# Kernel tuning notes

Hardware: AMD Instinct MI355X
Metric: run time of the kernel (lower is better)

The kernel has to match this reference:

```python
import jax, jax.numpy as jnp
import numpy as np

N_NODES = 50000
N_EDGES = 800000
FEAT_DIM = 1024
EMBED_DIM = 128


def setup_inputs() -> dict:
    key = jax.random.key(0)
    k_x, k_w, k_r, k_c, k_v = jax.random.split(key, 5)
    x = jax.random.normal(k_x, (N_NODES, FEAT_DIM), dtype=jnp.float32)
    # xavier-uniform equivalent for weight [embed_dim, feat_dim]
    limit = float(np.sqrt(6.0 / (EMBED_DIM + FEAT_DIM)))
    weight = jax.random.uniform(k_w, (EMBED_DIM, FEAT_DIM), dtype=jnp.float32,
                                minval=-limit, maxval=limit)
    # sparse adjacency in COO form (row = destination, col = source)
    adj_row = jax.random.randint(k_r, (N_EDGES,), 0, N_NODES, dtype=jnp.int32)
    adj_col = jax.random.randint(k_c, (N_EDGES,), 0, N_NODES, dtype=jnp.int32)
    adj_vals = jax.random.uniform(k_v, (N_EDGES,), dtype=jnp.float32)
    return {"x": x, "weight": weight, "adj_row": adj_row,
            "adj_col": adj_col, "adj_vals": adj_vals}


def reference(x, weight, adj_row, adj_col, adj_vals):
    # Fused GeMM-SpMM: out = A @ (x @ W^T)
    h = jnp.einsum('nf,ef->ne', x, weight)          # [N, embed_dim] dense GEMM
    msgs = adj_vals[:, None] * h[adj_col]           # gather source rows, scale by edge weight
    out = jax.ops.segment_sum(msgs, adj_row, num_segments=N_NODES)  # scatter-add to dest rows
    return out
```

## Files before the change

### kernel.cpp

```cpp
#include <hip/hip_runtime.h>
#include <hip/hip_bf16.h>

#define FEAT 1024
#define EMBED 128
#define CAP 64
#define OVF_CAP 4096

typedef __attribute__((ext_vector_type(8))) short short8;
typedef __attribute__((ext_vector_type(4))) float floatx4;

__device__ inline ushort f2bf(float f) {
    __hip_bfloat16 h = __float2bfloat16(f);
    return *reinterpret_cast<ushort*>(&h);
}
__device__ inline float bfbits_lo(uint u) {
    uint v = u << 16; return *reinterpret_cast<float*>(&v);
}
__device__ inline float bfbits_hi(uint u) {
    uint v = u & 0xffff0000u; return *reinterpret_cast<float*>(&v);
}

__device__ inline void async_copy16(const void* g, void* l) {
    __builtin_amdgcn_global_load_lds(
        (const __attribute__((address_space(1))) void*)g,
        (__attribute__((address_space(3))) void*)l, 16, 0, 0);
}

__global__ void swizzle_weight_kernel(const float* __restrict__ w,
                                      ushort* __restrict__ wbs) {
    int gid = blockIdx.x * blockDim.x + threadIdx.x;
    int l = gid & 63;
    int t = (gid >> 6) & 7;
    int s = gid >> 9;
    int row = t * 16 + (l & 15);
    int col = s * 32 + (l >> 4) * 8;
    const float* src = w + (size_t)row * FEAT + col;
    float4 v0 = *(const float4*)(src);
    float4 v1 = *(const float4*)(src + 4);
    short8 o;
    o[0] = f2bf(v0.x); o[1] = f2bf(v0.y); o[2] = f2bf(v0.z); o[3] = f2bf(v0.w);
    o[4] = f2bf(v1.x); o[5] = f2bf(v1.y); o[6] = f2bf(v1.z); o[7] = f2bf(v1.w);
    *(short8*)(wbs + (size_t)gid * 8) = o;
}

__launch_bounds__(256, 2)
__global__ void gemm_bucket_kernel(const float* __restrict__ x,
                                   const ushort* __restrict__ wbs,
                                   ushort* __restrict__ hb, int n_nodes,
                                   const int* __restrict__ adj_row,
                                   const int* __restrict__ adj_col,
                                   const float* __restrict__ adj_vals,
                                   int* __restrict__ cnt,
                                   int2* __restrict__ bucket,
                                   int* __restrict__ ovf_cnt,
                                   int* __restrict__ ovf_list,
                                   int n_edges, int gemm_blocks) {
    __shared__ ushort lds[2][16384];

    if (blockIdx.x >= gemm_blocks) {
        int e = (blockIdx.x - gemm_blocks) * 256 + threadIdx.x;
        if (e < n_edges) {
            int r = adj_row[e];
            int slot = atomicAdd(&cnt[r], 1);
            if (slot < CAP) {
                bucket[(size_t)r * CAP + slot] =
                    make_int2(adj_col[e], __float_as_int(adj_vals[e]));
            } else {
                int oi = atomicAdd(ovf_cnt, 1);
                if (oi < OVF_CAP) ovf_list[oi] = e;
            }
        }
        return;
    }

    const int lane = threadIdx.x & 63;
    const int wave = threadIdx.x >> 6;
    const int q    = lane >> 4;
    const int m    = lane & 15;
    const int base = blockIdx.x * 128 + wave * 32;

    int row0 = base + m;
    int row1 = base + 16 + m;
    int r0l = row0 < n_nodes ? row0 : (n_nodes - 1);
    int r1l = row1 < n_nodes ? row1 : (n_nodes - 1);
    const float* xp0 = x + (size_t)r0l * FEAT + q * 8;
    const float* xp1 = x + (size_t)r1l * FEAT + q * 8;

    const char* wb = (const char*)wbs;
    const size_t stage_src_off = (size_t)(wave * 8 * 64 + lane) * 16;
    const int    stage_dst_off = wave * 8192;

    {
        const char* src = wb + stage_src_off;
        char* dst = (char*)lds[0] + stage_dst_off;
#pragma unroll
        for (int k = 0; k < 8; ++k)
            async_copy16(src + k * 1024, dst + k * 1024);
    }

    float4 A[4][4];
#pragma unroll
    for (int u = 0; u < 4; ++u) {
        A[u][0] = *(const float4*)(xp0 + u * 32);
        A[u][1] = *(const float4*)(xp0 + u * 32 + 4);
        A[u][2] = *(const float4*)(xp1 + u * 32);
        A[u][3] = *(const float4*)(xp1 + u * 32 + 4);
    }

    floatx4 acc[2][8];
#pragma unroll
    for (int rf = 0; rf < 2; ++rf)
#pragma unroll
        for (int t = 0; t < 8; ++t) acc[rf][t] = (floatx4)(0.0f);

    __syncthreads();

    for (int c = 0; c < 8; ++c) {
        const ushort* buf = lds[c & 1];
        if (c < 7) {
            const char* src = wb + (size_t)(c + 1) * 32768 + stage_src_off;
            char* dst = (char*)lds[(c + 1) & 1] + stage_dst_off;
#pragma unroll
            for (int k = 0; k < 8; ++k)
                async_copy16(src + k * 1024, dst + k * 1024);
        }
#pragma unroll
        for (int u = 0; u < 4; ++u) {
            const ushort* bs = buf + u * 4096 + lane * 8;
            short8 bf[8];
#pragma unroll
            for (int t = 0; t < 8; ++t) bf[t] = *(const short8*)(bs + t * 512);

            short8 af0, af1;
            af0[0] = f2bf(A[u][0].x); af0[1] = f2bf(A[u][0].y);
            af0[2] = f2bf(A[u][0].z); af0[3] = f2bf(A[u][0].w);
            af0[4] = f2bf(A[u][1].x); af0[5] = f2bf(A[u][1].y);
            af0[6] = f2bf(A[u][1].z); af0[7] = f2bf(A[u][1].w);
            af1[0] = f2bf(A[u][2].x); af1[1] = f2bf(A[u][2].y);
            af1[2] = f2bf(A[u][2].z); af1[3] = f2bf(A[u][2].w);
            af1[4] = f2bf(A[u][3].x); af1[5] = f2bf(A[u][3].y);
            af1[6] = f2bf(A[u][3].z); af1[7] = f2bf(A[u][3].w);

            if (c < 7) {
                const float* p0 = xp0 + (c + 1) * 128;
                const float* p1 = xp1 + (c + 1) * 128;
                if (u == 1) {
#pragma unroll
                    for (int uu = 0; uu < 2; ++uu) {
                        A[uu][0] = *(const float4*)(p0 + uu * 32);
                        A[uu][1] = *(const float4*)(p0 + uu * 32 + 4);
                        A[uu][2] = *(const float4*)(p1 + uu * 32);
                        A[uu][3] = *(const float4*)(p1 + uu * 32 + 4);
                    }
                } else if (u == 3) {
#pragma unroll
                    for (int uu = 2; uu < 4; ++uu) {
                        A[uu][0] = *(const float4*)(p0 + uu * 32);
                        A[uu][1] = *(const float4*)(p0 + uu * 32 + 4);
                        A[uu][2] = *(const float4*)(p1 + uu * 32);
                        A[uu][3] = *(const float4*)(p1 + uu * 32 + 4);
                    }
                }
            }
#pragma unroll
            for (int t = 0; t < 8; ++t) {
                acc[0][t] = __builtin_amdgcn_mfma_f32_16x16x32_bf16(af0, bf[t], acc[0][t], 0, 0, 0);
                acc[1][t] = __builtin_amdgcn_mfma_f32_16x16x32_bf16(af1, bf[t], acc[1][t], 0, 0, 0);
            }
        }
        __syncthreads();
    }

#pragma unroll
    for (int rf = 0; rf < 2; ++rf) {
#pragma unroll
        for (int t = 0; t < 8; ++t) {
#pragma unroll
            for (int r = 0; r < 4; ++r) {
                int rr = base + rf * 16 + q * 4 + r;
                if (rr < n_nodes)
                    hb[(size_t)rr * EMBED + t * 16 + m] = f2bf(acc[rf][t][r]);
            }
        }
    }
}

__launch_bounds__(256)
__global__ void gather_kernel(const int* __restrict__ cnt,
                              const int2* __restrict__ bucket,
                              const ushort* __restrict__ hb,
                              const int* __restrict__ ovf_cnt,
                              const int* __restrict__ ovf_list,
                              const int* __restrict__ adj_row,
                              const int* __restrict__ adj_col,
                              const float* __restrict__ adj_vals,
                              float* __restrict__ out, int n_nodes) {
    int node = __builtin_amdgcn_readfirstlane(blockIdx.x * 4 + (threadIdx.x >> 6));
    if (node >= n_nodes) return;
    int lane = threadIdx.x & 63;
    int c_raw = cnt[node];
    int c = c_raw > CAP ? CAP : c_raw;
    const int2* bp = bucket + (size_t)node * CAP;
    const ushort* hl = hb + lane * 2;

    float accx = 0.0f, accy = 0.0f;
    int j = 0;
    for (; j + 8 <= c; j += 8) {
        int4 e01 = *(const int4*)(bp + j);
        int4 e23 = *(const int4*)(bp + j + 2);
        int4 e45 = *(const int4*)(bp + j + 4);
        int4 e67 = *(const int4*)(bp + j + 6);
        uint u0 = *(const uint*)(hl + (size_t)e01.x * EMBED);
        uint u1 = *(const uint*)(hl + (size_t)e01.z * EMBED);
        uint u2 = *(const uint*)(hl + (size_t)e23.x * EMBED);
        uint u3 = *(const uint*)(hl + (size_t)e23.z * EMBED);
        uint u4 = *(const uint*)(hl + (size_t)e45.x * EMBED);
        uint u5 = *(const uint*)(hl + (size_t)e45.z * EMBED);
        uint u6 = *(const uint*)(hl + (size_t)e67.x * EMBED);
        uint u7 = *(const uint*)(hl + (size_t)e67.z * EMBED);
        float w0 = __int_as_float(e01.y), w1 = __int_as_float(e01.w);
        float w2 = __int_as_float(e23.y), w3 = __int_as_float(e23.w);
        float w4 = __int_as_float(e45.y), w5 = __int_as_float(e45.w);
        float w6 = __int_as_float(e67.y), w7 = __int_as_float(e67.w);
        accx = fmaf(w0, bfbits_lo(u0), accx);  accy = fmaf(w0, bfbits_hi(u0), accy);
        accx = fmaf(w1, bfbits_lo(u1), accx);  accy = fmaf(w1, bfbits_hi(u1), accy);
        accx = fmaf(w2, bfbits_lo(u2), accx);  accy = fmaf(w2, bfbits_hi(u2), accy);
        accx = fmaf(w3, bfbits_lo(u3), accx);  accy = fmaf(w3, bfbits_hi(u3), accy);
        accx = fmaf(w4, bfbits_lo(u4), accx);  accy = fmaf(w4, bfbits_hi(u4), accy);
        accx = fmaf(w5, bfbits_lo(u5), accx);  accy = fmaf(w5, bfbits_hi(u5), accy);
        accx = fmaf(w6, bfbits_lo(u6), accx);  accy = fmaf(w6, bfbits_hi(u6), accy);
        accx = fmaf(w7, bfbits_lo(u7), accx);  accy = fmaf(w7, bfbits_hi(u7), accy);
    }
    for (; j + 2 <= c; j += 2) {
        int4 e01 = *(const int4*)(bp + j);
        uint u0 = *(const uint*)(hl + (size_t)e01.x * EMBED);
        uint u1 = *(const uint*)(hl + (size_t)e01.z * EMBED);
        float w0 = __int_as_float(e01.y), w1 = __int_as_float(e01.w);
        accx = fmaf(w0, bfbits_lo(u0), accx);  accy = fmaf(w0, bfbits_hi(u0), accy);
        accx = fmaf(w1, bfbits_lo(u1), accx);  accy = fmaf(w1, bfbits_hi(u1), accy);
    }
    if (j < c) {
        int2 ev = bp[j];
        uint u = *(const uint*)(hl + (size_t)ev.x * EMBED);
        float w = __int_as_float(ev.y);
        accx = fmaf(w, bfbits_lo(u), accx);
        accy = fmaf(w, bfbits_hi(u), accy);
    }
    if (c_raw > CAP) {
        int n = *ovf_cnt;
        if (n > OVF_CAP) n = OVF_CAP;
        for (int i = 0; i < n; ++i) {
            int e = ovf_list[i];
            if (adj_row[e] == node) {
                uint u = *(const uint*)(hl + (size_t)adj_col[e] * EMBED);
                float w = adj_vals[e];
                accx = fmaf(w, bfbits_lo(u), accx);
                accy = fmaf(w, bfbits_hi(u), accy);
            }
        }
    }
    *(float2*)(out + (size_t)node * EMBED + lane * 2) = make_float2(accx, accy);
}

extern "C" void kernel_launch(void* const* d_in, const int* in_sizes, int n_in,
                              void* d_out, int out_size, void* d_ws, size_t ws_size,
                              hipStream_t stream) {
    const float* x        = (const float*)d_in[0];
    const float* w        = (const float*)d_in[1];
    const int*   adj_row  = (const int*)d_in[2];
    const int*   adj_col  = (const int*)d_in[3];
    const float* adj_vals = (const float*)d_in[4];

    const int n_nodes = in_sizes[0] / FEAT;
    const int n_edges = in_sizes[2];
    float* out = (float*)d_out;

    char* ws = (char*)d_ws;
    ushort* wbs = (ushort*)ws;
    size_t off = 262144;
    ushort* hb = (ushort*)(ws + off);
    off += (size_t)n_nodes * EMBED * sizeof(ushort);
    char* meta = ws + off;
    int* cnt      = (int*)meta;
    int* ovf_cnt  = (int*)(meta + (size_t)n_nodes * 4);
    int* ovf_list = ovf_cnt + 1;
    size_t meta_bytes = ((size_t)n_nodes * 4 + 4 + OVF_CAP * 4 + 15) & ~(size_t)15;
    int2* bucket = (int2*)(meta + meta_bytes);

    hipMemsetAsync(meta, 0, meta_bytes, stream);

    swizzle_weight_kernel<<<64, 256, 0, stream>>>(w, wbs);

    const int gemm_blocks   = (n_nodes + 127) / 128;
    const int bucket_blocks = (n_edges + 255) / 256;
    gemm_bucket_kernel<<<gemm_blocks + bucket_blocks, 256, 0, stream>>>(
        x, wbs, hb, n_nodes,
        adj_row, adj_col, adj_vals,
        cnt, bucket, ovf_cnt, ovf_list, n_edges, gemm_blocks);

    gather_kernel<<<(n_nodes + 3) / 4, 256, 0, stream>>>(
        cnt, bucket, hb, ovf_cnt, ovf_list, adj_row, adj_col, adj_vals,
        out, n_nodes);
}
```

Baseline: 365.9 us.

## Stage x and W via async LDS triple buffer, grid-stride bucketing, batched gather loads

The GEMM now streams both the fp32 x tiles and the bf16 weight chunks into LDS with async global-to-LDS copies. It uses a three-deep buffer with manual vmcnt waits and barriers, and XOR swizzling to avoid bank conflicts. This replaces per-thread register prefetch of x, and occupancy drops to one block per CU because of the 144KB LDS footprint. Edge bucketing switches to a fixed 512-block grid-stride loop, and the gather kernel processes 16 edges per batch with the next batch's edge descriptors prefetched.

```diff
diff --git a/kernel.cpp b/kernel.cpp
--- a/kernel.cpp
+++ b/kernel.cpp
@@ -5,6 +5,12 @@
 #define EMBED 128
 #define CAP 64
 #define OVF_CAP 4096
+
+#define NCH 16
+#define A_BYTES 32768
+#define B_BYTES 16384
+#define BUF_BYTES 49152
+#define NBUF 3
 
 typedef __attribute__((ext_vector_type(8))) short short8;
 typedef __attribute__((ext_vector_type(4))) float floatx4;
@@ -43,7 +49,7 @@
     *(short8*)(wbs + (size_t)gid * 8) = o;
 }
 
-__launch_bounds__(256, 2)
+__launch_bounds__(256, 1)
 __global__ void gemm_bucket_kernel(const float* __restrict__ x,
                                    const ushort* __restrict__ wbs,
                                    ushort* __restrict__ hb, int n_nodes,
@@ -54,12 +60,13 @@
                                    int2* __restrict__ bucket,
                                    int* __restrict__ ovf_cnt,
                                    int* __restrict__ ovf_list,
-                                   int n_edges, int gemm_blocks) {
-    __shared__ ushort lds[2][16384];
+                                   int n_edges, int gemm_blocks, int bucket_blocks) {
+    __shared__ __align__(16) char lds[NBUF * BUF_BYTES];
 
     if (blockIdx.x >= gemm_blocks) {
-        int e = (blockIdx.x - gemm_blocks) * 256 + threadIdx.x;
-        if (e < n_edges) {
+        int stride = bucket_blocks * 256;
+        for (int e = (blockIdx.x - gemm_blocks) * 256 + threadIdx.x;
+             e < n_edges; e += stride) {
             int r = adj_row[e];
             int slot = atomicAdd(&cnt[r], 1);
             if (slot < CAP) {
@@ -78,34 +85,33 @@
     const int q    = lane >> 4;
     const int m    = lane & 15;
     const int base = blockIdx.x * 128 + wave * 32;
-
-    int row0 = base + m;
-    int row1 = base + 16 + m;
-    int r0l = row0 < n_nodes ? row0 : (n_nodes - 1);
-    int r1l = row1 < n_nodes ? row1 : (n_nodes - 1);
-    const float* xp0 = x + (size_t)r0l * FEAT + q * 8;
-    const float* xp1 = x + (size_t)r1l * FEAT + q * 8;
-
-    const char* wb = (const char*)wbs;
-    const size_t stage_src_off = (size_t)(wave * 8 * 64 + lane) * 16;
-    const int    stage_dst_off = wave * 8192;
-
-    {
-        const char* src = wb + stage_src_off;
-        char* dst = (char*)lds[0] + stage_dst_off;
-#pragma unroll
-        for (int k = 0; k < 8; ++k)
-            async_copy16(src + k * 1024, dst + k * 1024);
-    }
-
-    float4 A[4][4];
-#pragma unroll
-    for (int u = 0; u < 4; ++u) {
-        A[u][0] = *(const float4*)(xp0 + u * 32);
-        A[u][1] = *(const float4*)(xp0 + u * 32 + 4);
-        A[u][2] = *(const float4*)(xp1 + u * 32);
-        A[u][3] = *(const float4*)(xp1 + u * 32 + 4);
-    }
+    const char* xb  = (const char*)x;
+    const char* wbb = (const char*)wbs;
+
+    size_t aoff[8];
+#pragma unroll
+    for (int k = 0; k < 8; ++k) {
+        int r   = k * 4 + (lane >> 4);
+        int row = base + r;
+        if (row >= n_nodes) row = n_nodes - 1;
+        int j = (lane & 15) ^ (r & 7);
+        aoff[k] = (size_t)row * (FEAT * 4) + (size_t)j * 16;
+    }
+
+#define STAGE(c_) do {                                                        \
+        char* buf_ = lds + ((c_) % NBUF) * BUF_BYTES;                         \
+        char* Aw_  = buf_ + wave * 8192;                                      \
+        _Pragma("unroll")                                                     \
+        for (int k = 0; k < 8; ++k)                                           \
+            async_copy16(xb + aoff[k] + (size_t)(c_) * 256, Aw_ + k * 1024);  \
+        const char* bs_ = wbb + (size_t)(c_) * B_BYTES + wave * 1024 + lane * 16; \
+        char* Bd_ = buf_ + A_BYTES + wave * 1024;                             \
+        _Pragma("unroll")                                                     \
+        for (int k = 0; k < 4; ++k)                                           \
+            async_copy16(bs_ + k * 4096, Bd_ + k * 4096);                     \
+    } while (0)
+
+    STAGE(0); STAGE(1); STAGE(2);
 
     floatx4 acc[2][8];
 #pragma unroll
@@ -113,63 +119,53 @@
 #pragma unroll
         for (int t = 0; t < 8; ++t) acc[rf][t] = (floatx4)(0.0f);
 
-    __syncthreads();
-
-    for (int c = 0; c < 8; ++c) {
-        const ushort* buf = lds[c & 1];
-        if (c < 7) {
-            const char* src = wb + (size_t)(c + 1) * 32768 + stage_src_off;
-            char* dst = (char*)lds[(c + 1) & 1] + stage_dst_off;
-#pragma unroll
-            for (int k = 0; k < 8; ++k)
-                async_copy16(src + k * 1024, dst + k * 1024);
-        }
-#pragma unroll
-        for (int u = 0; u < 4; ++u) {
-            const ushort* bs = buf + u * 4096 + lane * 8;
+    const int sw = (m & 7);
+    for (int c = 0; c < NCH; ++c) {
+        if (c <= NCH - 3)      asm volatile("s_waitcnt vmcnt(24)" ::: "memory");
+        else if (c == NCH - 2) asm volatile("s_waitcnt vmcnt(12)" ::: "memory");
+        else                   asm volatile("s_waitcnt vmcnt(0)"  ::: "memory");
+        __builtin_amdgcn_sched_barrier(0);
+        __builtin_amdgcn_s_barrier();
+        __builtin_amdgcn_sched_barrier(0);
+
+        const char* buf = lds + (c % NBUF) * BUF_BYTES;
+        const char* Aw  = buf + wave * 8192;
+        const char* Bb  = buf + A_BYTES;
+#pragma unroll
+        for (int s01 = 0; s01 < 2; ++s01) {
+            int slot0 = s01 * 8 + q * 2;
+            float4 a0l = *(const float4*)(Aw + m * 256 + ((slot0     ^ sw) * 16));
+            float4 a0h = *(const float4*)(Aw + m * 256 + (((slot0+1) ^ sw) * 16));
+            float4 a1l = *(const float4*)(Aw + (m+16) * 256 + ((slot0     ^ sw) * 16));
+            float4 a1h = *(const float4*)(Aw + (m+16) * 256 + (((slot0+1) ^ sw) * 16));
+
+            const char* bsrc = Bb + s01 * 8192 + lane * 16;
             short8 bf[8];
 #pragma unroll
-            for (int t = 0; t < 8; ++t) bf[t] = *(const short8*)(bs + t * 512);
+            for (int t = 0; t < 8; ++t) bf[t] = *(const short8*)(bsrc + t * 1024);
 
             short8 af0, af1;
-            af0[0] = f2bf(A[u][0].x); af0[1] = f2bf(A[u][0].y);
-            af0[2] = f2bf(A[u][0].z); af0[3] = f2bf(A[u][0].w);
-            af0[4] = f2bf(A[u][1].x); af0[5] = f2bf(A[u][1].y);
-            af0[6] = f2bf(A[u][1].z); af0[7] = f2bf(A[u][1].w);
-            af1[0] = f2bf(A[u][2].x); af1[1] = f2bf(A[u][2].y);
-            af1[2] = f2bf(A[u][2].z); af1[3] = f2bf(A[u][2].w);
-            af1[4] = f2bf(A[u][3].x); af1[5] = f2bf(A[u][3].y);
-            af1[6] = f2bf(A[u][3].z); af1[7] = f2bf(A[u][3].w);
-
-            if (c < 7) {
-                const float* p0 = xp0 + (c + 1) * 128;
-                const float* p1 = xp1 + (c + 1) * 128;
-                if (u == 1) {
-#pragma unroll
-                    for (int uu = 0; uu < 2; ++uu) {
-                        A[uu][0] = *(const float4*)(p0 + uu * 32);
-                        A[uu][1] = *(const float4*)(p0 + uu * 32 + 4);
-                        A[uu][2] = *(const float4*)(p1 + uu * 32);
-                        A[uu][3] = *(const float4*)(p1 + uu * 32 + 4);
-                    }
-                } else if (u == 3) {
-#pragma unroll
-                    for (int uu = 2; uu < 4; ++uu) {
-                        A[uu][0] = *(const float4*)(p0 + uu * 32);
-                        A[uu][1] = *(const float4*)(p0 + uu * 32 + 4);
-                        A[uu][2] = *(const float4*)(p1 + uu * 32);
-                        A[uu][3] = *(const float4*)(p1 + uu * 32 + 4);
-                    }
-                }
-            }
+            af0[0] = f2bf(a0l.x); af0[1] = f2bf(a0l.y);
+            af0[2] = f2bf(a0l.z); af0[3] = f2bf(a0l.w);
+            af0[4] = f2bf(a0h.x); af0[5] = f2bf(a0h.y);
+            af0[6] = f2bf(a0h.z); af0[7] = f2bf(a0h.w);
+            af1[0] = f2bf(a1l.x); af1[1] = f2bf(a1l.y);
+            af1[2] = f2bf(a1l.z); af1[3] = f2bf(a1l.w);
+            af1[4] = f2bf(a1h.x); af1[5] = f2bf(a1h.y);
+            af1[6] = f2bf(a1h.z); af1[7] = f2bf(a1h.w);
+
 #pragma unroll
             for (int t = 0; t < 8; ++t) {
                 acc[0][t] = __builtin_amdgcn_mfma_f32_16x16x32_bf16(af0, bf[t], acc[0][t], 0, 0, 0);
                 acc[1][t] = __builtin_amdgcn_mfma_f32_16x16x32_bf16(af1, bf[t], acc[1][t], 0, 0, 0);
             }
         }
-        __syncthreads();
-    }
+
+        __builtin_amdgcn_s_barrier();
+        __builtin_amdgcn_sched_barrier(0);
+        if (c <= NCH - 4) STAGE(c + 3);
+    }
+#undef STAGE
 
 #pragma unroll
     for (int rf = 0; rf < 2; ++rf) {
@@ -204,33 +200,33 @@
     const ushort* hl = hb + lane * 2;
 
     float accx = 0.0f, accy = 0.0f;
-    int j = 0;
-    for (; j + 8 <= c; j += 8) {
-        int4 e01 = *(const int4*)(bp + j);
-        int4 e23 = *(const int4*)(bp + j + 2);
-        int4 e45 = *(const int4*)(bp + j + 4);
-        int4 e67 = *(const int4*)(bp + j + 6);
-        uint u0 = *(const uint*)(hl + (size_t)e01.x * EMBED);
-        uint u1 = *(const uint*)(hl + (size_t)e01.z * EMBED);
-        uint u2 = *(const uint*)(hl + (size_t)e23.x * EMBED);
-        uint u3 = *(const uint*)(hl + (size_t)e23.z * EMBED);
-        uint u4 = *(const uint*)(hl + (size_t)e45.x * EMBED);
-        uint u5 = *(const uint*)(hl + (size_t)e45.z * EMBED);
-        uint u6 = *(const uint*)(hl + (size_t)e67.x * EMBED);
-        uint u7 = *(const uint*)(hl + (size_t)e67.z * EMBED);
-        float w0 = __int_as_float(e01.y), w1 = __int_as_float(e01.w);
-        float w2 = __int_as_float(e23.y), w3 = __int_as_float(e23.w);
-        float w4 = __int_as_float(e45.y), w5 = __int_as_float(e45.w);
-        float w6 = __int_as_float(e67.y), w7 = __int_as_float(e67.w);
-        accx = fmaf(w0, bfbits_lo(u0), accx);  accy = fmaf(w0, bfbits_hi(u0), accy);
-        accx = fmaf(w1, bfbits_lo(u1), accx);  accy = fmaf(w1, bfbits_hi(u1), accy);
-        accx = fmaf(w2, bfbits_lo(u2), accx);  accy = fmaf(w2, bfbits_hi(u2), accy);
-        accx = fmaf(w3, bfbits_lo(u3), accx);  accy = fmaf(w3, bfbits_hi(u3), accy);
-        accx = fmaf(w4, bfbits_lo(u4), accx);  accy = fmaf(w4, bfbits_hi(u4), accy);
-        accx = fmaf(w5, bfbits_lo(u5), accx);  accy = fmaf(w5, bfbits_hi(u5), accy);
-        accx = fmaf(w6, bfbits_lo(u6), accx);  accy = fmaf(w6, bfbits_hi(u6), accy);
-        accx = fmaf(w7, bfbits_lo(u7), accx);  accy = fmaf(w7, bfbits_hi(u7), accy);
-    }
+    int nb = c >> 4;
+    if (nb > 0) {
+        int4 eb[8];
+#pragma unroll
+        for (int i = 0; i < 8; ++i) eb[i] = *(const int4*)(bp + i * 2);
+        for (int b = 0; b < nb; ++b) {
+            uint u[16]; float wv[16];
+#pragma unroll
+            for (int i = 0; i < 8; ++i) {
+                u[2*i]   = *(const uint*)(hl + (size_t)eb[i].x * EMBED);
+                u[2*i+1] = *(const uint*)(hl + (size_t)eb[i].z * EMBED);
+                wv[2*i]   = __int_as_float(eb[i].y);
+                wv[2*i+1] = __int_as_float(eb[i].w);
+            }
+            if (b + 1 < nb) {
+#pragma unroll
+                for (int i = 0; i < 8; ++i)
+                    eb[i] = *(const int4*)(bp + (b + 1) * 16 + i * 2);
+            }
+#pragma unroll
+            for (int i = 0; i < 16; ++i) {
+                accx = fmaf(wv[i], bfbits_lo(u[i]), accx);
+                accy = fmaf(wv[i], bfbits_hi(u[i]), accy);
+            }
+        }
+    }
+    int j = nb * 16;
     for (; j + 2 <= c; j += 2) {
         int4 e01 = *(const int4*)(bp + j);
         uint u0 = *(const uint*)(hl + (size_t)e01.x * EMBED);
@@ -292,11 +288,11 @@
     swizzle_weight_kernel<<<64, 256, 0, stream>>>(w, wbs);
 
     const int gemm_blocks   = (n_nodes + 127) / 128;
-    const int bucket_blocks = (n_edges + 255) / 256;
+    const int bucket_blocks = 512;
     gemm_bucket_kernel<<<gemm_blocks + bucket_blocks, 256, 0, stream>>>(
         x, wbs, hb, n_nodes,
         adj_row, adj_col, adj_vals,
-        cnt, bucket, ovf_cnt, ovf_list, n_edges, gemm_blocks);
+        cnt, bucket, ovf_cnt, ovf_list, n_edges, gemm_blocks, bucket_blocks);
 
     gather_kernel<<<(n_nodes + 3) / 4, 256, 0, stream>>>(
         cnt, bucket, hb, ovf_cnt, ovf_list, adj_row, adj_col, adj_vals,
```

Measured after the change: 385.4 us. 1.05x slower.
